# Performance work log

Hardware: AMD Instinct MI355X
Metric: run time of the kernel (lower is better)

Reference implementation:

```python
import jax, jax.numpy as jnp
import numpy as np
from jax import lax

FPS_NUM, K = 2048, 32


def fps_subsample(x, n):
    # x: [B, N, 3] -> [B, n, 3]; farthest point sampling, deterministic start at index 0
    B, N, _ = x.shape
    d0 = jnp.sum((x - x[:, :1]) ** 2, axis=-1)  # [B, N] dist to point 0

    def step(dists, _):
        nxt = jnp.argmax(dists, axis=1)                       # [B]
        p = x[jnp.arange(B), nxt]                             # [B, 3]
        dists = jnp.minimum(dists, jnp.sum((x - p[:, None]) ** 2, axis=-1))
        return dists, nxt

    _, idxs = lax.scan(step, d0, None, length=n - 1)          # [n-1, B]
    idxs = jnp.concatenate([jnp.zeros((1, B), jnp.int32), idxs.astype(jnp.int32)], axis=0).T  # [B, n]
    return x[jnp.arange(B)[:, None], idxs]                    # [B, n, 3]


def knn_idx(x, k):
    # x: [B, C, N] -> [B, N, k] indices of k nearest neighbors in feature space
    xx = jnp.sum(x * x, axis=1)                               # [B, N]
    inner = jnp.einsum('bcn,bcm->bnm', x, x)
    neg_dist = 2.0 * inner - xx[:, :, None] - xx[:, None, :]  # -||xi-xj||^2
    return lax.top_k(neg_dist, k)[1]


def get_graph_feature(x, k):
    # DGCNN edge features: x [B, C, N] -> [B, 2C, N, k]
    B, C, N = x.shape
    idx = knn_idx(x, k)                                       # [B, N, k]
    xt = jnp.transpose(x, (0, 2, 1))                          # [B, N, C]
    nbr = xt[jnp.arange(B)[:, None, None], idx]               # [B, N, k, C]
    ctr = jnp.broadcast_to(xt[:, :, None], nbr.shape)
    feat = jnp.concatenate([nbr - ctr, ctr], axis=-1)         # [B, N, k, 2C]
    return jnp.transpose(feat, (0, 3, 1, 2))


def attention(xq, xk, pos, Wq, bq, Wk, bk, Wv, bv, Wp, bp):
    # positional attention over k neighbors: xq/xk [B, Cin, N, k], pos [B, 3, N] -> [B, dim, N]
    q = jnp.einsum('bcnk,dc->bdnk', xq, Wq) + bq[:, None, None]
    kk = jnp.einsum('bcnk,dc->bdnk', xk, Wk) + bk[:, None, None]
    v = jnp.einsum('bcnk,dc->bdnk', xk, Wv) + bv[:, None, None]
    p = jnp.einsum('bcn,dc->bdn', pos, Wp) + bp[:, None]      # [B, dim, N]
    dim = Wq.shape[0]
    logits = jnp.einsum('bdnk,bdnk->bnk', q, kk) / jnp.sqrt(jnp.float32(dim))
    attn = jax.nn.softmax(logits, axis=-1)                    # [B, N, k]
    return jnp.einsum('bnk,bdnk->bdn', attn, v + p[:, :, :, None])


def _layer_params(key, cin, dim):
    ks = jax.random.split(key, 4)
    s = 1.0 / np.sqrt(cin)
    return (jax.random.normal(ks[0], (dim, cin), jnp.float32) * s,
            jnp.zeros((dim,), jnp.float32),
            jax.random.normal(ks[1], (dim, cin), jnp.float32) * s,
            jnp.zeros((dim,), jnp.float32),
            jax.random.normal(ks[2], (dim, cin), jnp.float32) * s,
            jnp.zeros((dim,), jnp.float32),
            jax.random.normal(ks[3], (dim, 3), jnp.float32) * (1.0 / np.sqrt(3.0)),
            jnp.zeros((dim,), jnp.float32))


def setup_inputs() -> dict:
    key = jax.random.key(0)
    kx, k1, k2, k3 = jax.random.split(key, 4)
    x = jax.random.normal(kx, (8, 16384, 3), jnp.float32)
    out = {'x': x}
    for name, kk_, cin, dim in (('t1', k1, 6, 64), ('t2', k2, 128, 64), ('t3', k3, 128, 128)):
        Wq, bq, Wk, bk, Wv, bv, Wp, bp = _layer_params(kk_, cin, dim)
        out.update({f'{name}_Wq': Wq, f'{name}_bq': bq, f'{name}_Wk': Wk, f'{name}_bk': bk,
                    f'{name}_Wv': Wv, f'{name}_bv': bv, f'{name}_Wp': Wp, f'{name}_bp': bp})
    return out


def reference(x, t1_Wq, t1_bq, t1_Wk, t1_bk, t1_Wv, t1_bv, t1_Wp, t1_bp,
              t2_Wq, t2_bq, t2_Wk, t2_bk, t2_Wv, t2_bv, t2_Wp, t2_bp,
              t3_Wq, t3_bq, t3_Wk, t3_bk, t3_Wv, t3_bv, t3_Wp, t3_bp):
    partial = jnp.transpose(fps_subsample(x, FPS_NUM), (0, 2, 1))       # [B, 3, n]
    g = get_graph_feature(partial, K)                                    # [B, 6, n, k]
    x1 = attention(g, g, partial, t1_Wq, t1_bq, t1_Wk, t1_bk, t1_Wv, t1_bv, t1_Wp, t1_bp)  # [B, 64, n]
    g = get_graph_feature(x1, K)                                         # [B, 128, n, k]
    x2 = attention(g, g, partial, t2_Wq, t2_bq, t2_Wk, t2_bk, t2_Wv, t2_bv, t2_Wp, t2_bp)  # [B, 64, n]
    g = get_graph_feature(x2, K)                                         # [B, 128, n, k]
    x3 = attention(g, g, partial, t3_Wq, t3_bq, t3_Wk, t3_bk, t3_Wv, t3_bv, t3_Wp, t3_bp)  # [B, 128, n]
    feats = jnp.concatenate([x1, x2, x3], axis=1)                        # [B, 256, n]
    return jnp.concatenate([jnp.max(feats, axis=-1), jnp.mean(feats, axis=-1)], axis=1)    # [B, 512]
```

## Files before the change

kernel.cpp:

```cpp
#include <hip/hip_runtime.h>
#include <math.h>

#define NB 8
#define NIN 16384
#define NP 2048
#define KNN 32
#define TOTPTS (NB * NP)

#define NEG_INF (-__builtin_inff())
#define POS_INF (__builtin_inff())

__device__ __forceinline__ float2 pk_add(float2 a, float2 b) {
  float2 d;
  asm("v_pk_add_f32 %0, %1, %2" : "=v"(d) : "v"(a), "v"(b));
  return d;
}
__device__ __forceinline__ float2 pk_mul(float2 a, float2 b) {
  float2 d;
  asm("v_pk_mul_f32 %0, %1, %2" : "=v"(d) : "v"(a), "v"(b));
  return d;
}

#define DPP_F(old, v, C, RM) \
  __int_as_float(__builtin_amdgcn_update_dpp(__float_as_int(old), __float_as_int(v), C, RM, 0xf, false))
#define DPP_I(old, v, C, RM) \
  __builtin_amdgcn_update_dpp(old, v, C, RM, 0xf, false)

__device__ __forceinline__ float wave_max_f(float v) {
  v = fmaxf(v, DPP_F(NEG_INF, v, 0x111, 0xf));
  v = fmaxf(v, DPP_F(NEG_INF, v, 0x112, 0xf));
  v = fmaxf(v, DPP_F(NEG_INF, v, 0x114, 0xf));
  v = fmaxf(v, DPP_F(NEG_INF, v, 0x118, 0xf));
  v = fmaxf(v, DPP_F(NEG_INF, v, 0x142, 0xa));
  v = fmaxf(v, DPP_F(NEG_INF, v, 0x143, 0xc));
  return v;
}
__device__ __forceinline__ int wave_min_i(int v) {
  v = min(v, DPP_I(0x7fffffff, v, 0x111, 0xf));
  v = min(v, DPP_I(0x7fffffff, v, 0x112, 0xf));
  v = min(v, DPP_I(0x7fffffff, v, 0x114, 0xf));
  v = min(v, DPP_I(0x7fffffff, v, 0x118, 0xf));
  v = min(v, DPP_I(0x7fffffff, v, 0x142, 0xa));
  v = min(v, DPP_I(0x7fffffff, v, 0x143, 0xc));
  return v;
}

__device__ __forceinline__ float readlane63f(float v) {
  return __int_as_float(__builtin_amdgcn_readlane(__float_as_int(v), 63));
}

__global__ __launch_bounds__(1024) void fps_kernel(const float* __restrict__ x,
                                                   float* __restrict__ partial) {
  const int b = blockIdx.x;
  const int t = threadIdx.x;
  const float* xb = x + (size_t)b * NIN * 3;
  float* pb = partial + (size_t)b * NP * 3;
  __shared__ unsigned long long skey[NP];
  for (int i = t; i < NP; i += 1024) skey[i] = 0ull;

  float2 px[8], py[8], pz[8], dd[8];
#pragma unroll
  for (int j = 0; j < 8; ++j) {
    const int i0 = (2 * j) * 1024 + t, i1 = (2 * j + 1) * 1024 + t;
    px[j] = make_float2(xb[3 * i0], xb[3 * i1]);
    py[j] = make_float2(xb[3 * i0 + 1], xb[3 * i1 + 1]);
    pz[j] = make_float2(xb[3 * i0 + 2], xb[3 * i1 + 2]);
  }
  const float qx0 = xb[0], qy0 = xb[1], qz0 = xb[2];
  if (t == 0) { pb[0] = qx0; pb[1] = qy0; pb[2] = qz0; }

  float bv = NEG_INF;
  int bi = 0;
  {
    const float2 nx2 = make_float2(-qx0, -qx0);
    const float2 ny2 = make_float2(-qy0, -qy0);
    const float2 nz2 = make_float2(-qz0, -qz0);
#pragma unroll
    for (int j = 0; j < 8; ++j) {
      float2 dx = pk_add(px[j], nx2), dy = pk_add(py[j], ny2), dz = pk_add(pz[j], nz2);
      float2 nd = pk_add(pk_add(pk_mul(dx, dx), pk_mul(dy, dy)), pk_mul(dz, dz));
      dd[j] = nd;
      if (nd.x > bv) { bv = nd.x; bi = (2 * j) * 1024 + t; }
      if (nd.y > bv) { bv = nd.y; bi = (2 * j + 1) * 1024 + t; }
    }
  }
  __syncthreads();

  for (int it = 1; it < NP; ++it) {
    const float wm = wave_max_f(bv);
    const float smax = readlane63f(wm);
    const int sel = (bv == smax) ? bi : 0x7fffffff;
    const int wi = wave_min_i(sel);
    if ((t & 63) == 63) {
      const unsigned long long key =
          ((unsigned long long)__float_as_uint(smax) << 32) | (unsigned int)(~wi);
      atomicMax(&skey[it], key);
    }
    __syncthreads();
    const unsigned long long gk = skey[it];
    const int gbi = (int)(~(unsigned int)gk);
    const int u = __builtin_amdgcn_readfirstlane(gbi);
    const float nqx = xb[3 * u], nqy = xb[3 * u + 1], nqz = xb[3 * u + 2];
    if (t == 0) { pb[3 * it] = nqx; pb[3 * it + 1] = nqy; pb[3 * it + 2] = nqz; }

    const float2 nx2 = make_float2(-nqx, -nqx);
    const float2 ny2 = make_float2(-nqy, -nqy);
    const float2 nz2 = make_float2(-nqz, -nqz);
    bv = NEG_INF;
    bi = 0;
#pragma unroll
    for (int j = 0; j < 8; ++j) {
      float2 dx = pk_add(px[j], nx2), dy = pk_add(py[j], ny2), dz = pk_add(pz[j], nz2);
      float2 nd = pk_add(pk_add(pk_mul(dx, dx), pk_mul(dy, dy)), pk_mul(dz, dz));
      const float a0 = fminf(dd[j].x, nd.x);
      dd[j].x = a0;
      if (a0 > bv) { bv = a0; bi = (2 * j) * 1024 + t; }
      const float a1 = fminf(dd[j].y, nd.y);
      dd[j].y = a1;
      if (a1 > bv) { bv = a1; bi = (2 * j + 1) * 1024 + t; }
    }
  }
}

__global__ void xx_kernel(const float* __restrict__ F, float* __restrict__ xxg, int C) {
  int i = blockIdx.x * 256 + threadIdx.x;
  if (i >= TOTPTS) return;
  const float* f = F + (size_t)i * C;
  float s = 0.f;
  for (int c = 0; c < C; ++c) s = __fadd_rn(s, __fmul_rn(f[c], f[c]));
  xxg[i] = s;
}

__global__ __launch_bounds__(1024) void knn3_kernel(const float* __restrict__ F,
                                                    int* __restrict__ idxg) {
  const int b = blockIdx.z;
  const int t = threadIdx.x;
  const int w = t >> 6, lane = t & 63;
  __shared__ float spx[NP], spy[NP], spz[NP], sxx[NP];
  const float* Fb = F + (size_t)b * NP * 3;
  for (int i = t; i < NP; i += 1024) {
    const float a0 = Fb[3 * i], a1 = Fb[3 * i + 1], a2 = Fb[3 * i + 2];
    spx[i] = a0; spy[i] = a1; spz[i] = a2;
    float s = __fadd_rn(0.f, __fmul_rn(a0, a0));
    s = __fadd_rn(s, __fmul_rn(a1, a1));
    s = __fadd_rn(s, __fmul_rn(a2, a2));
    sxx[i] = s;
  }
  __syncthreads();
  const int row = blockIdx.x * 16 + w;
  const float a0 = spx[row], a1 = spy[row], a2 = spz[row];
  const float xn = sxx[row];
  float v[32];
#pragma unroll
  for (int s = 0; s < 32; ++s) {
    const int m = s * 64 + lane;
    float acc = fmaf(a0, spx[m], 0.f);
    acc = fmaf(a1, spy[m], acc);
    acc = fmaf(a2, spz[m], acc);
    v[s] = __fsub_rn(__fsub_rn(2.0f * acc, xn), sxx[m]);
  }
  int* out = idxg + ((size_t)b * NP + row) * KNN;
  for (int tt = 0; tt < KNN; ++tt) {
    float bv = v[0];
    int bs = 0;
#pragma unroll
    for (int s = 1; s < 32; ++s) {
      if (v[s] > bv) { bv = v[s]; bs = s; }
    }
    int bi = bs * 64 + lane;
    const float vmax = readlane63f(wave_max_f(bv));
    const int sel = (bv == vmax) ? bi : 0x7fffffff;
    const int wbi = __builtin_amdgcn_readlane(wave_min_i(sel), 63);
    if (lane == 0) out[tt] = wbi;
    const bool own = (lane == (wbi & 63));
    const int cs = wbi >> 6;
#pragma unroll
    for (int s = 0; s < 32; ++s)
      if (own && s == cs) v[s] = NEG_INF;
  }
}

template <int C>
__global__ __launch_bounds__(256) void dist_gemm(const float* __restrict__ F,
                                                 const float* __restrict__ xxg,
                                                 float* __restrict__ D, int bofs) {
  __shared__ float As[64][C + 1];
  __shared__ float Bs[64][C + 1];
  const int b = bofs + blockIdx.z;
  float* Ds = D + (size_t)blockIdx.z * NP * NP;
  const int tid = threadIdx.x;
  const int n0 = blockIdx.y * 64, m0 = blockIdx.x * 64;
  const float* Fb = F + (size_t)b * NP * C;
  const float* xxb = xxg + b * NP;
  for (int t = tid; t < 64 * C; t += 256) {
    int r = t / C, c = t - r * C;
    As[r][c] = Fb[(size_t)(n0 + r) * C + c];
    Bs[r][c] = Fb[(size_t)(m0 + r) * C + c];
  }
  __syncthreads();
  const int tx = tid & 15, ty = tid >> 4;
  float acc[4][4] = {};
  for (int c = 0; c < C; ++c) {
    float a[4], bb[4];
#pragma unroll
    for (int i = 0; i < 4; ++i) a[i] = As[ty * 4 + i][c];
#pragma unroll
    for (int j = 0; j < 4; ++j) bb[j] = Bs[tx * 4 + j][c];
#pragma unroll
    for (int i = 0; i < 4; ++i)
#pragma unroll
      for (int j = 0; j < 4; ++j) acc[i][j] = fmaf(a[i], bb[j], acc[i][j]);
  }
#pragma unroll
  for (int i = 0; i < 4; ++i) {
    int n = n0 + ty * 4 + i;
    float xn = xxb[n];
    float4 o;
    o.x = __fsub_rn(__fsub_rn(2.0f * acc[i][0], xn), xxb[m0 + tx * 4 + 0]);
    o.y = __fsub_rn(__fsub_rn(2.0f * acc[i][1], xn), xxb[m0 + tx * 4 + 1]);
    o.z = __fsub_rn(__fsub_rn(2.0f * acc[i][2], xn), xxb[m0 + tx * 4 + 2]);
    o.w = __fsub_rn(__fsub_rn(2.0f * acc[i][3], xn), xxb[m0 + tx * 4 + 3]);
    *(float4*)&Ds[(size_t)n * NP + m0 + tx * 4] = o;
  }
}

__global__ __launch_bounds__(256) void select_kernel(const float* __restrict__ D,
                                                     int* __restrict__ idxg, int bofs) {
  const int lane = threadIdx.x & 63;
  const int b = bofs + blockIdx.z;
  const int row = blockIdx.x * 4 + (threadIdx.x >> 6);
  const float* Drow = D + (size_t)blockIdx.z * NP * NP + (size_t)row * NP;
  float v[32];
#pragma unroll
  for (int s = 0; s < 32; ++s) v[s] = Drow[s * 64 + lane];
  int* out = idxg + ((size_t)b * NP + row) * KNN;
  for (int t = 0; t < KNN; ++t) {
    float bv = v[0];
    int bs = 0;
#pragma unroll
    for (int s = 1; s < 32; ++s) {
      if (v[s] > bv) { bv = v[s]; bs = s; }
    }
    int bi = bs * 64 + lane;
    const float vmax = readlane63f(wave_max_f(bv));
    const int sel = (bv == vmax) ? bi : 0x7fffffff;
    const int wbi = __builtin_amdgcn_readlane(wave_min_i(sel), 63);
    if (lane == 0) out[t] = wbi;
    const bool own = (lane == (wbi & 63));
    const int cs = wbi >> 6;
#pragma unroll
    for (int s = 0; s < 32; ++s)
      if (own && s == cs) v[s] = NEG_INF;
  }
}

template <int C, int DIM>
__global__ __launch_bounds__(256) void proj_kernel(
    const float* __restrict__ F, const float* __restrict__ pos,
    const float* __restrict__ Wq, const float* __restrict__ bq,
    const float* __restrict__ Wk, const float* __restrict__ bk,
    const float* __restrict__ Wv, const float* __restrict__ bv,
    const float* __restrict__ Wp, const float* __restrict__ bp,
    float* __restrict__ Uq, float* __restrict__ Uk, float* __restrict__ Uv,
    float* __restrict__ Uqc, float* __restrict__ Ukc, float* __restrict__ W6) {
  constexpr int PTS = 16;
  constexpr int GROUPS = 256 / DIM;
  constexpr int PPT = PTS / GROUPS;
  __shared__ float xs[PTS][C];
  __shared__ float ps[PTS][3];
  const int tid = threadIdx.x;
  const int base = blockIdx.x * PTS;
  for (int t = tid; t < PTS * C; t += 256) {
    int r = t / C;
    xs[r][t - r * C] = F[(size_t)(base + r) * C + (t - r * C)];
  }
  for (int t = tid; t < PTS * 3; t += 256) {
    int r = t / 3;
    ps[r][t - r * 3] = pos[(size_t)(base + r) * 3 + (t - r * 3)];
  }
  __syncthreads();
  const int g = tid / DIM;
  const int d = tid - g * DIM;
  float uq[PPT], uqd[PPT], uk[PPT], ukd[PPT], uv[PPT], uvd[PPT];
#pragma unroll
  for (int p = 0; p < PPT; ++p) { uq[p] = uqd[p] = uk[p] = ukd[p] = uv[p] = uvd[p] = 0.f; }
  const float* wqr = Wq + (size_t)d * (2 * C);
  const float* wkr = Wk + (size_t)d * (2 * C);
  const float* wvr = Wv + (size_t)d * (2 * C);
  for (int c = 0; c < C; ++c) {
    const float wq1 = wqr[c], wqd_ = wqr[C + c] - wq1;
    const float wk1 = wkr[c], wkd_ = wkr[C + c] - wk1;
    const float wv1 = wvr[c], wvd_ = wvr[C + c] - wv1;
#pragma unroll
    for (int p = 0; p < PPT; ++p) {
      const float xc = xs[g + p * GROUPS][c];
      uq[p] = fmaf(wq1, xc, uq[p]);
      uqd[p] = fmaf(wqd_, xc, uqd[p]);
      uk[p] = fmaf(wk1, xc, uk[p]);
      ukd[p] = fmaf(wkd_, xc, ukd[p]);
      uv[p] = fmaf(wv1, xc, uv[p]);
      uvd[p] = fmaf(wvd_, xc, uvd[p]);
    }
  }
  const float bqd = bq[d], bkd = bk[d], bvd = bv[d];
  const float wp0 = Wp[d * 3], wp1 = Wp[d * 3 + 1], wp2 = Wp[d * 3 + 2], bpd = bp[d];
#pragma unroll
  for (int p = 0; p < PPT; ++p) {
    const int lp = g + p * GROUPS;
    const size_t o = (size_t)(base + lp) * DIM + d;
    const float pd = wp0 * ps[lp][0] + wp1 * ps[lp][1] + wp2 * ps[lp][2] + bpd;
    Uq[o] = uq[p];
    Uqc[o] = uqd[p] + bqd;
    Uk[o] = uk[p];
    Ukc[o] = ukd[p] + bkd;
    Uv[o] = uv[p];
    W6[o] = uvd[p] + bvd + pd;
  }
}

template <int DIM>
__global__ void prep_kernel(const float* __restrict__ Wq, const float* __restrict__ bq,
                            const float* __restrict__ Wk, const float* __restrict__ bk,
                            const float* __restrict__ Wv, const float* __restrict__ bv,
                            float* __restrict__ Wcat, float* __restrict__ bcat) {
  const int o = blockIdx.x * 256 + threadIdx.x;
  constexpr int ND = 6 * DIM;
  if (o >= ND) return;
  const int blk = o / DIM, d = o % DIM;
  bcat[o] = (blk == 1) ? bq[d] : (blk == 3) ? bk[d] : (blk == 5) ? bv[d] : 0.f;
  const float* W = (blk < 2) ? Wq : (blk < 4) ? Wk : Wv;
  for (int c = 0; c < 64; ++c) {
    const float w1 = W[(size_t)d * 128 + c];
    const float w2 = W[(size_t)d * 128 + 64 + c];
    Wcat[(size_t)c * ND + o] = (blk & 1) ? (w2 - w1) : w1;
  }
}

template <int DIM>
__global__ void pos_kernel(const float* __restrict__ pos, const float* __restrict__ Wp,
                           const float* __restrict__ bp, float* __restrict__ P) {
  const int idx = blockIdx.x * 256 + threadIdx.x;
  const int pt = idx / DIM, d = idx - pt * DIM;
  P[idx] = Wp[d * 3] * pos[pt * 3] + Wp[d * 3 + 1] * pos[pt * 3 + 1] +
           Wp[d * 3 + 2] * pos[pt * 3 + 2] + bp[d];
}

template <int DIM>
__global__ __launch_bounds__(256) void gemm_proj(
    const float* __restrict__ F, const float* __restrict__ Wcat,
    const float* __restrict__ bcat, const float* __restrict__ P,
    float* __restrict__ Uq, float* __restrict__ Uqc, float* __restrict__ Uk,
    float* __restrict__ Ukc, float* __restrict__ Uv, float* __restrict__ W6) {
  constexpr int ND = 6 * DIM;
  __shared__ float As[64][65];
  __shared__ float Bs[64][65];
  const int tid = threadIdx.x;
  const int p0 = blockIdx.x * 64;
  const int n0 = blockIdx.y * 64;
  {
    const int r0 = tid >> 4, c4 = (tid & 15) * 4;
    for (int r = r0; r < 64; r += 16) {
      float4 a = *(const float4*)&F[(size_t)(p0 + r) * 64 + c4];
      As[r][c4] = a.x; As[r][c4 + 1] = a.y; As[r][c4 + 2] = a.z; As[r][c4 + 3] = a.w;
      float4 bb = *(const float4*)&Wcat[(size_t)r * ND + n0 + c4];
      Bs[r][c4] = bb.x; Bs[r][c4 + 1] = bb.y; Bs[r][c4 + 2] = bb.z; Bs[r][c4 + 3] = bb.w;
    }
  }
  __syncthreads();
  const int tx = tid & 15, ty = tid >> 4;
  float acc[4][4] = {};
#pragma unroll 4
  for (int c = 0; c < 64; ++c) {
    float a[4], bb[4];
#pragma unroll
    for (int i = 0; i < 4; ++i) a[i] = As[ty * 4 + i][c];
#pragma unroll
    for (int j = 0; j < 4; ++j) bb[j] = Bs[c][tx * 4 + j];
#pragma unroll
    for (int i = 0; i < 4; ++i)
#pragma unroll
      for (int j = 0; j < 4; ++j) acc[i][j] = fmaf(a[i], bb[j], acc[i][j]);
  }
  const int obuf = n0 / DIM;
  const int oloc = n0 - obuf * DIM;
  float* outp = (obuf == 0) ? Uq : (obuf == 1) ? Uqc : (obuf == 2) ? Uk
              : (obuf == 3) ? Ukc : (obuf == 4) ? Uv : W6;
  const float b0 = bcat[n0 + tx * 4], b1 = bcat[n0 + tx * 4 + 1];
  const float b2 = bcat[n0 + tx * 4 + 2], b3 = bcat[n0 + tx * 4 + 3];
#pragma unroll
  for (int i = 0; i < 4; ++i) {
    const int p = p0 + ty * 4 + i;
    float4 r = make_float4(acc[i][0] + b0, acc[i][1] + b1, acc[i][2] + b2, acc[i][3] + b3);
    if (obuf == 5) {
      float4 pv = *(const float4*)&P[(size_t)p * DIM + oloc + tx * 4];
      r.x += pv.x; r.y += pv.y; r.z += pv.z; r.w += pv.w;
    }
    *(float4*)&outp[(size_t)p * DIM + oloc + tx * 4] = r;
  }
}

template <int DIM>
__global__ __launch_bounds__(256) void attn_kernel(
    const float* __restrict__ Uq, const float* __restrict__ Uk, const float* __restrict__ Uv,
    const float* __restrict__ Uqc, const float* __restrict__ Ukc, const float* __restrict__ W6g,
    const int* __restrict__ idxg, float* __restrict__ outF) {
  const int w = threadIdx.x >> 6, lane = threadIdx.x & 63;
  const int pt = blockIdx.x * 4 + w;
  const int b = pt >> 11;
  __shared__ int sidx[4][KNN];
  __shared__ float sqc[4][DIM], skc[4][DIM], sw6[4][DIM];
  __shared__ float sattn[4][KNN];
  const size_t rowo = (size_t)pt * DIM;
  if (lane < KNN) sidx[w][lane] = idxg[(size_t)pt * KNN + lane];
  for (int d = lane; d < DIM; d += 64) {
    sqc[w][d] = Uqc[rowo + d];
    skc[w][d] = Ukc[rowo + d];
    sw6[w][d] = W6g[rowo + d];
  }
  __syncthreads();
  {
    const int kk = lane & 31;
    const int h = lane >> 5;
    const int ik = sidx[w][kk];
    const float* qr = Uq + (size_t)(b * NP + ik) * DIM;
    const float* kr = Uk + (size_t)(b * NP + ik) * DIM;
    float lg = 0.f;
    const int d0 = h * (DIM / 2), d1 = d0 + DIM / 2;
    for (int d = d0; d < d1; d += 4) {
      float4 qa = *(const float4*)(qr + d);
      float4 ka = *(const float4*)(kr + d);
      float4 qc = *(const float4*)(&sqc[w][d]);
      float4 kc = *(const float4*)(&skc[w][d]);
      lg += (qa.x + qc.x) * (ka.x + kc.x);
      lg += (qa.y + qc.y) * (ka.y + kc.y);
      lg += (qa.z + qc.z) * (ka.z + kc.z);
      lg += (qa.w + qc.w) * (ka.w + kc.w);
    }
    lg += __shfl_xor(lg, 32);
    lg *= (DIM == 64) ? 0.125f : 0.08838834764831845f;
    float m = lg;
#pragma unroll
    for (int off = 16; off; off >>= 1) m = fmaxf(m, __shfl_xor(m, off));
    float e = expf(lg - m);
    float s = e;
#pragma unroll
    for (int off = 16; off; off >>= 1) s += __shfl_xor(s, off);
    if (lane < KNN) sattn[w][lane] = e / s;
  }
  __syncthreads();
  float acc[DIM / 64];
#pragma unroll
  for (int q = 0; q < DIM / 64; ++q) acc[q] = 0.f;
  for (int k = 0; k < KNN; ++k) {
    const int ik = sidx[w][k];
    const float a = sattn[w][k];
    const float* vr = Uv + (size_t)(b * NP + ik) * DIM;
#pragma unroll
    for (int q = 0; q < DIM / 64; ++q) {
      const int d = q * 64 + lane;
      acc[q] = fmaf(a, vr[d] + sw6[w][d], acc[q]);
    }
  }
#pragma unroll
  for (int q = 0; q < DIM / 64; ++q) outF[rowo + q * 64 + lane] = acc[q];
}

__global__ __launch_bounds__(256) void pool_kernel(const float* __restrict__ x1,
                                                   const float* __restrict__ x2,
                                                   const float* __restrict__ x3,
                                                   float* __restrict__ out) {
  const int b = blockIdx.x, c = threadIdx.x;
  const float* src;
  int dim, cl;
  if (c < 64) {
    src = x1 + (size_t)b * NP * 64; dim = 64; cl = c;
  } else if (c < 128) {
    src = x2 + (size_t)b * NP * 64; dim = 64; cl = c - 64;
  } else {
    src = x3 + (size_t)b * NP * 128; dim = 128; cl = c - 128;
  }
  float mx = NEG_INF, sm = 0.f;
#pragma unroll 8
  for (int n = 0; n < NP; ++n) {
    float v = src[(size_t)n * dim + cl];
    mx = fmaxf(mx, v);
    sm += v;
  }
  out[b * 512 + c] = mx;
  out[b * 512 + 256 + c] = sm * (1.0f / 2048.0f);
}

extern "C" void kernel_launch(void* const* d_in, const int* in_sizes, int n_in,
                              void* d_out, int out_size, void* d_ws, size_t ws_size,
                              hipStream_t stream) {
  const float* x = (const float*)d_in[0];
  const float* W[24];
  for (int i = 0; i < 24; ++i) W[i] = (const float*)d_in[1 + i];

  float* ws = (float*)d_ws;
  size_t off = 0;
  float* partial = ws + off; off += (size_t)NB * NP * 3;
  float* xxbuf = ws + off;   off += TOTPTS;
  int* idxb = (int*)(ws + off); off += (size_t)TOTPTS * KNN;
  float* x1 = ws + off; off += (size_t)TOTPTS * 64;
  float* x2 = ws + off; off += (size_t)TOTPTS * 64;
  float* x3 = ws + off; off += (size_t)TOTPTS * 128;
  float* Uq = ws + off;  off += (size_t)TOTPTS * 128;
  float* Uk = ws + off;  off += (size_t)TOTPTS * 128;
  float* Uv = ws + off;  off += (size_t)TOTPTS * 128;
  float* Uqc = ws + off; off += (size_t)TOTPTS * 128;
  float* Ukc = ws + off; off += (size_t)TOTPTS * 128;
  float* W6 = ws + off;  off += (size_t)TOTPTS * 128;
  float* Pbuf = ws + off; off += (size_t)TOTPTS * 128;
  float* Wcat = ws + off; off += (size_t)64 * 768;
  float* bcat = ws + off; off += 768;
  if (ws_size < off * sizeof(float)) return;

  float* Dbig = ws + off;
  const size_t need_big = (off + (size_t)NB * NP * NP) * sizeof(float);
  const bool bigws = (ws_size >= need_big);
  float* D = bigws ? Dbig : Uq;
  const int NZ = bigws ? NB : 1;

  fps_kernel<<<NB, 1024, 0, stream>>>(x, partial);

  knn3_kernel<<<dim3(NP / 16, 1, NB), 1024, 0, stream>>>(partial, idxb);
  proj_kernel<3, 64><<<TOTPTS / 16, 256, 0, stream>>>(
      partial, partial, W[0], W[1], W[2], W[3], W[4], W[5], W[6], W[7],
      Uq, Uk, Uv, Uqc, Ukc, W6);
  attn_kernel<64><<<TOTPTS / 4, 256, 0, stream>>>(Uq, Uk, Uv, Uqc, Ukc, W6, idxb, x1);

  xx_kernel<<<TOTPTS / 256, 256, 0, stream>>>(x1, xxbuf, 64);
  for (int b = 0; b < NB; b += NZ) {
    dist_gemm<64><<<dim3(32, 32, NZ), 256, 0, stream>>>(x1, xxbuf, D, b);
    select_kernel<<<dim3(NP / 4, 1, NZ), 256, 0, stream>>>(D, idxb, b);
  }
  prep_kernel<64><<<2, 256, 0, stream>>>(W[8], W[9], W[10], W[11], W[12], W[13], Wcat, bcat);
  pos_kernel<64><<<TOTPTS * 64 / 256, 256, 0, stream>>>(partial, W[14], W[15], Pbuf);
  gemm_proj<64><<<dim3(TOTPTS / 64, 6), 256, 0, stream>>>(
      x1, Wcat, bcat, Pbuf, Uq, Uqc, Uk, Ukc, Uv, W6);
  attn_kernel<64><<<TOTPTS / 4, 256, 0, stream>>>(Uq, Uk, Uv, Uqc, Ukc, W6, idxb, x2);

  xx_kernel<<<TOTPTS / 256, 256, 0, stream>>>(x2, xxbuf, 64);
  for (int b = 0; b < NB; b += NZ) {
    dist_gemm<64><<<dim3(32, 32, NZ), 256, 0, stream>>>(x2, xxbuf, D, b);
    select_kernel<<<dim3(NP / 4, 1, NZ), 256, 0, stream>>>(D, idxb, b);
  }
  prep_kernel<128><<<3, 256, 0, stream>>>(W[16], W[17], W[18], W[19], W[20], W[21], Wcat, bcat);
  pos_kernel<128><<<TOTPTS * 128 / 256, 256, 0, stream>>>(partial, W[22], W[23], Pbuf);
  gemm_proj<128><<<dim3(TOTPTS / 64, 12), 256, 0, stream>>>(
      x2, Wcat, bcat, Pbuf, Uq, Uqc, Uk, Ukc, Uv, W6);
  attn_kernel<128><<<TOTPTS / 4, 256, 0, stream>>>(Uq, Uk, Uv, Uqc, Ukc, W6, idxb, x3);

  pool_kernel<<<NB, 256, 0, stream>>>(x1, x2, x3, (float*)d_out);
}
```

Before: 4.719 ms.

## Restructure FPS loop to one barrier with per-wave candidate coords; split pooling

The FPS loop now runs the wave-level argmax at the end of each iteration. Each wave stores its candidate's coordinates in a double-buffered shared slot, and two atomic keys per step cut contention. After the barrier every thread reads the winner's coordinates from shared memory instead of loading them from global memory, which takes a dependent global load off the serial critical path. Separately, the final pooling is split into a chunked partial-reduction kernel plus a combine kernel to expose more parallelism than 8 blocks.

Result: faster. 4.472 ms (-5.2%).

```diff
diff --git a/kernel.cpp b/kernel.cpp
--- a/kernel.cpp
+++ b/kernel.cpp
@@ -53,10 +53,12 @@
                                                    float* __restrict__ partial) {
   const int b = blockIdx.x;
   const int t = threadIdx.x;
+  const int w = t >> 6, l = t & 63;
   const float* xb = x + (size_t)b * NIN * 3;
   float* pb = partial + (size_t)b * NP * 3;
-  __shared__ unsigned long long skey[NP];
-  for (int i = t; i < NP; i += 1024) skey[i] = 0ull;
+  __shared__ unsigned long long skey[NP][2];
+  __shared__ float4 swave[2][16];
+  for (int i = t; i < NP; i += 1024) { skey[i][0] = 0ull; skey[i][1] = 0ull; }
 
   float2 px[8], py[8], pz[8], dd[8];
 #pragma unroll
@@ -84,23 +86,29 @@
       if (nd.y > bv) { bv = nd.y; bi = (2 * j + 1) * 1024 + t; }
     }
   }
+
+  {
+    const float wm = wave_max_f(bv);
+    const float smaxw = readlane63f(wm);
+    const int sel = (bv == smaxw) ? bi : 0x7fffffff;
+    const int wiw = __builtin_amdgcn_readlane(wave_min_i(sel), 63);
+    const float ax = xb[3 * wiw], ay = xb[3 * wiw + 1], az = xb[3 * wiw + 2];
+    if (l == 63) {
+      const unsigned long long key =
+          ((unsigned long long)__float_as_uint(smaxw) << 32) | (unsigned int)(~wiw);
+      atomicMax(&skey[1][w & 1], key);
+    }
+    if (l == 0) swave[1 & 1][w] = make_float4(ax, ay, az, 0.f);
+  }
   __syncthreads();
 
   for (int it = 1; it < NP; ++it) {
-    const float wm = wave_max_f(bv);
-    const float smax = readlane63f(wm);
-    const int sel = (bv == smax) ? bi : 0x7fffffff;
-    const int wi = wave_min_i(sel);
-    if ((t & 63) == 63) {
-      const unsigned long long key =
-          ((unsigned long long)__float_as_uint(smax) << 32) | (unsigned int)(~wi);
-      atomicMax(&skey[it], key);
-    }
-    __syncthreads();
-    const unsigned long long gk = skey[it];
+    const unsigned long long k0 = skey[it][0], k1 = skey[it][1];
+    const unsigned long long gk = (k0 > k1) ? k0 : k1;
     const int gbi = (int)(~(unsigned int)gk);
-    const int u = __builtin_amdgcn_readfirstlane(gbi);
-    const float nqx = xb[3 * u], nqy = xb[3 * u + 1], nqz = xb[3 * u + 2];
+    const int wstar = (gbi >> 6) & 15;
+    const float4 qc = swave[it & 1][wstar];
+    const float nqx = qc.x, nqy = qc.y, nqz = qc.z;
     if (t == 0) { pb[3 * it] = nqx; pb[3 * it + 1] = nqy; pb[3 * it + 2] = nqz; }
 
     const float2 nx2 = make_float2(-nqx, -nqx);
@@ -119,6 +127,21 @@
       dd[j].y = a1;
       if (a1 > bv) { bv = a1; bi = (2 * j + 1) * 1024 + t; }
     }
+
+    if (it + 1 < NP) {
+      const float wm = wave_max_f(bv);
+      const float smaxw = readlane63f(wm);
+      const int sel = (bv == smaxw) ? bi : 0x7fffffff;
+      const int wiw = __builtin_amdgcn_readlane(wave_min_i(sel), 63);
+      const float ax = xb[3 * wiw], ay = xb[3 * wiw + 1], az = xb[3 * wiw + 2];
+      if (l == 63) {
+        const unsigned long long key =
+            ((unsigned long long)__float_as_uint(smaxw) << 32) | (unsigned int)(~wiw);
+        atomicMax(&skey[it + 1][w & 1], key);
+      }
+      if (l == 0) swave[(it + 1) & 1][w] = make_float4(ax, ay, az, 0.f);
+    }
+    __syncthreads();
   }
 }
 
@@ -465,11 +488,13 @@
   for (int q = 0; q < DIM / 64; ++q) outF[rowo + q * 64 + lane] = acc[q];
 }
 
-__global__ __launch_bounds__(256) void pool_kernel(const float* __restrict__ x1,
-                                                   const float* __restrict__ x2,
-                                                   const float* __restrict__ x3,
-                                                   float* __restrict__ out) {
-  const int b = blockIdx.x, c = threadIdx.x;
+#define PCHUNKS 16
+__global__ __launch_bounds__(256) void pool1_kernel(const float* __restrict__ x1,
+                                                    const float* __restrict__ x2,
+                                                    const float* __restrict__ x3,
+                                                    float* __restrict__ pmax,
+                                                    float* __restrict__ psum) {
+  const int b = blockIdx.x, ch = blockIdx.y, c = threadIdx.x;
   const float* src;
   int dim, cl;
   if (c < 64) {
@@ -479,12 +504,29 @@
   } else {
     src = x3 + (size_t)b * NP * 128; dim = 128; cl = c - 128;
   }
+  const int n0 = ch * (NP / PCHUNKS), n1 = n0 + NP / PCHUNKS;
   float mx = NEG_INF, sm = 0.f;
 #pragma unroll 8
-  for (int n = 0; n < NP; ++n) {
+  for (int n = n0; n < n1; ++n) {
     float v = src[(size_t)n * dim + cl];
     mx = fmaxf(mx, v);
     sm += v;
+  }
+  const size_t o = ((size_t)b * PCHUNKS + ch) * 256 + c;
+  pmax[o] = mx;
+  psum[o] = sm;
+}
+
+__global__ __launch_bounds__(256) void pool2_kernel(const float* __restrict__ pmax,
+                                                    const float* __restrict__ psum,
+                                                    float* __restrict__ out) {
+  const int b = blockIdx.x, c = threadIdx.x;
+  float mx = NEG_INF, sm = 0.f;
+#pragma unroll
+  for (int ch = 0; ch < PCHUNKS; ++ch) {
+    const size_t o = ((size_t)b * PCHUNKS + ch) * 256 + c;
+    mx = fmaxf(mx, pmax[o]);
+    sm += psum[o];
   }
   out[b * 512 + c] = mx;
   out[b * 512 + 256 + c] = sm * (1.0f / 2048.0f);
@@ -514,6 +556,8 @@
   float* Pbuf = ws + off; off += (size_t)TOTPTS * 128;
   float* Wcat = ws + off; off += (size_t)64 * 768;
   float* bcat = ws + off; off += 768;
+  float* pmax = ws + off; off += (size_t)NB * PCHUNKS * 256;
+  float* psum = ws + off; off += (size_t)NB * PCHUNKS * 256;
   if (ws_size < off * sizeof(float)) return;
 
   float* Dbig = ws + off;
@@ -552,5 +596,6 @@
       x2, Wcat, bcat, Pbuf, Uq, Uqc, Uk, Ukc, Uv, W6);
   attn_kernel<128><<<TOTPTS / 4, 256, 0, stream>>>(Uq, Uk, Uv, Uqc, Ukc, W6, idxb, x3);
 
-  pool_kernel<<<NB, 256, 0, stream>>>(x1, x2, x3, (float*)d_out);
-}
+  pool1_kernel<<<dim3(NB, PCHUNKS), 256, 0, stream>>>(x1, x2, x3, pmax, psum);
+  pool2_kernel<<<NB, 256, 0, stream>>>(pmax, psum, (float*)d_out);
+}
```
